# Optimization experiments

Measured on AMD Instinct MI355X. Metric: run time of the kernel, lower is better.

Reference implementation:

```python
import jax, jax.numpy as jnp
import numpy as np

H = 4          # num_heads
EPS = 1e-3     # BatchNorm eps


def conv1x1(x, W, b):
    # x: [B, Cin, N], W: [Cout, Cin], b: [Cout]
    return jnp.einsum('oi,bin->bon', W, x) + b[None, :, None]


def setup_inputs() -> dict:
    key = jax.random.key(0)
    ks = jax.random.split(key, 20)
    B, D, N = 8, 256, 2048
    s = 0.05
    inp = {
        'x': jax.random.normal(ks[0], (B, D, N), jnp.float32),
        'source': jax.random.normal(ks[1], (B, D, N), jnp.float32),
        # attention projections (Conv1d k=1 -> [out, in] weight + bias)
        'Wq': jax.random.normal(ks[2], (D, D), jnp.float32) * s,
        'bq': jax.random.normal(ks[3], (D,), jnp.float32) * s,
        'Wk': jax.random.normal(ks[4], (D, D), jnp.float32) * s,
        'bk': jax.random.normal(ks[5], (D,), jnp.float32) * s,
        'Wv': jax.random.normal(ks[6], (D, D), jnp.float32) * s,
        'bv': jax.random.normal(ks[7], (D,), jnp.float32) * s,
        'Wm': jax.random.normal(ks[8], (D, D), jnp.float32) * s,
        'bm': jax.random.normal(ks[9], (D,), jnp.float32) * s,
        # MLP: [2D -> 2D (BN+ReLU) -> D]
        'W1': jax.random.normal(ks[10], (2 * D, 2 * D), jnp.float32) * s,
        'b1': jax.random.normal(ks[11], (2 * D,), jnp.float32) * s,
        'gamma1': jnp.ones((2 * D,), jnp.float32),
        'beta1': jnp.zeros((2 * D,), jnp.float32),
        'W2': jax.random.normal(ks[12], (D, 2 * D), jnp.float32) * s,
        'b2': jnp.zeros((D,), jnp.float32),  # init.constant_(bias, 0)
    }
    return inp


def reference(x, source, Wq, bq, Wk, bk, Wv, bv, Wm, bm, W1, b1, gamma1, beta1, W2, b2):
    B, D, N = x.shape
    hd = D // H  # head dim; torch view splits channels as (hd, H)
    q = conv1x1(x, Wq, bq).reshape(B, hd, H, N)
    k = conv1x1(source, Wk, bk).reshape(B, hd, H, -1)
    v = conv1x1(source, Wv, bv).reshape(B, hd, H, -1)
    scores = jnp.einsum('bdhn,bdhm->bhnm', q, k) / jnp.sqrt(jnp.float32(hd))
    prob = jax.nn.softmax(scores, axis=-1)
    attn = jnp.einsum('bhnm,bdhm->bdhn', prob, v).reshape(B, D, N)
    message = conv1x1(attn, Wm, bm)
    # MLP on concat([x, message])
    h = conv1x1(jnp.concatenate([x, message], axis=1), W1, b1)  # [B, 2D, N]
    mean = jnp.mean(h, axis=(0, 2), keepdims=True)
    var = jnp.mean((h - mean) ** 2, axis=(0, 2), keepdims=True)  # biased (BN training)
    h = (h - mean) / jnp.sqrt(var + EPS)
    h = h * gamma1[None, :, None] + beta1[None, :, None]
    h = jax.nn.relu(h)
    out = conv1x1(h, W2, b2)  # [B, D, N]
    return out
```

## Files before the change

kernel.cpp:

```cpp
#include <hip/hip_runtime.h>
#include <hip/hip_bf16.h>
#include <math.h>

typedef __bf16 bf16;
typedef __bf16 bf16x4 __attribute__((ext_vector_type(4)));
typedef __bf16 bf16x8 __attribute__((ext_vector_type(8)));
typedef float f32x4 __attribute__((ext_vector_type(4)));

static constexpr int N_TOK = 2048;
static constexpr int B_SZ = 8;

#define MFMA(a, b, c) __builtin_amdgcn_mfma_f32_16x16x32_bf16((a), (b), (c), 0, 0, 0)

__device__ __forceinline__ float fast_exp2(float x) {
  float r;
  asm("v_exp_f32 %0, %1" : "=v"(r) : "v"(x));
  return r;
}

__device__ __host__ __forceinline__ int pi_fwd(int d) {
  return (d & 32) | ((d & 12) << 1) | ((d & 16) >> 2) | (d & 3);
}
__device__ __forceinline__ int pi_inv(int p) {
  return (p & 32) | ((p & 4) << 2) | ((p & 24) >> 1) | (p & 3);
}

__device__ __forceinline__ bf16x4 lo4(bf16x8 v) {
  return __builtin_shufflevector(v, v, 0, 1, 2, 3);
}
__device__ __forceinline__ bf16x4 hi4(bf16x8 v) {
  return __builtin_shufflevector(v, v, 4, 5, 6, 7);
}

__global__ __launch_bounds__(256) void transpose_cvt2(const float* __restrict__ x,
                                                      const float* __restrict__ src,
                                                      bf16* __restrict__ xT,
                                                      bf16* __restrict__ sT) {
  const int z = blockIdx.z;
  const float* in = (z < 8) ? x : src;
  bf16* outT = (z < 8) ? xT : sT;
  const int b = z & 7;
  const int n0 = blockIdx.x * 64, c0 = blockIdx.y * 64;
  const int t = threadIdx.x;
  __shared__ bf16 T[64][72];
  {
    int c = t >> 2, nc = (t & 3) * 16;
    const float* s = in + ((long)b * 256 + c0 + c) * N_TOK + n0 + nc;
#pragma unroll
    for (int q = 0; q < 4; ++q) {
      float4 v = *(const float4*)(s + q * 4);
      T[c][nc + q * 4 + 0] = (bf16)v.x;
      T[c][nc + q * 4 + 1] = (bf16)v.y;
      T[c][nc + q * 4 + 2] = (bf16)v.z;
      T[c][nc + q * 4 + 3] = (bf16)v.w;
    }
  }
  __syncthreads();
  {
    int n = t >> 2, cc = (t & 3) * 16;
    bf16x8 o0, o1;
#pragma unroll
    for (int j = 0; j < 8; ++j) { o0[j] = T[cc + j][n]; o1[j] = T[cc + 8 + j][n]; }
    bf16* dst = outT + ((long)b * N_TOK + n0 + n) * 256 + c0 + cc;
    *(bf16x8*)dst = o0;
    *(bf16x8*)(dst + 8) = o1;
  }
}

__global__ void prep_kernel(const float* __restrict__ Wq, const float* __restrict__ Wk,
                            const float* __restrict__ Wv, const float* __restrict__ Wm,
                            const float* __restrict__ W1, const float* __restrict__ W2,
                            const float* __restrict__ bq, const float* __restrict__ bk,
                            const float* __restrict__ bv,
                            bf16* __restrict__ Wqkv, bf16* __restrict__ Wmp,
                            bf16* __restrict__ W1b, bf16* __restrict__ W2b,
                            float* __restrict__ bqkv) {
  const float SCL = 0.125f * 1.44269504088896340736f;
  int i = blockIdx.x * 256 + threadIdx.x;
  if (i < 65536) {
    int cp = i >> 8, k = i & 255;
    int hh = cp >> 6, pp = cp & 63;
    int d = pi_inv(pp);
    int srcQK = (d * 4 + hh) * 256 + k;
    Wqkv[i] = (bf16)(Wq[srcQK] * SCL);
    Wqkv[65536 + i] = (bf16)Wk[srcQK];
    int srcV = (((cp & 63) << 2) | (cp >> 6)) * 256 + k;
    Wqkv[131072 + i] = (bf16)Wv[srcV];
    int m = i >> 8, c2 = i & 255;
    Wmp[i] = (bf16)Wm[m * 256 + (((c2 & 63) << 2) | (c2 >> 6))];
  } else if (i < 65536 + 262144) {
    int j = i - 65536;
    W1b[j] = (bf16)W1[j];
  } else if (i < 65536 + 262144 + 131072) {
    int j = i - 327680;
    W2b[j] = (bf16)W2[j];
  } else if (i < 65536 + 262144 + 131072 + 256) {
    int c2 = i - 458752;
    int hh = c2 >> 6, pp = c2 & 63;
    int d = pi_inv(pp);
    bqkv[c2] = bq[d * 4 + hh] * SCL;
    bqkv[256 + c2] = bk[d * 4 + hh];
    bqkv[512 + c2] = bv[(c2 & 63) * 4 + (c2 >> 6)];
  }
}

template <int TJ, int MODE>
__global__ __launch_bounds__(256) void gemm_t(
    const bf16* __restrict__ A0, const bf16* __restrict__ A1, int cSplit,
    const bf16* __restrict__ B, long batchB,
    const float* __restrict__ bias, const float2* __restrict__ bnSS,
    bf16* __restrict__ outK, bf16* __restrict__ outV,
    const float2* __restrict__ mlp,
    void* __restrict__ outp, long outR, long batchOut, int K,
    float* __restrict__ psOut, float* __restrict__ pssOut) {
  const int j0 = blockIdx.x * TJ;
  const int i0 = blockIdx.y * 128;
  const int b = blockIdx.z;
  const int t = threadIdx.x;
  const int lane = t & 63, w = t >> 6;
  const int wi = (w >> 1) * 64;
  const int wj = (w & 1) * (TJ / 2);
  const int nl = lane & 15, g = lane >> 4;
  constexpr int FN = TJ / 32;
  constexpr int AsE = 2 * 128 * 40;
  constexpr int BsE = 2 * TJ * 40;
  __shared__ bf16 smem[AsE + BsE];
  auto As = reinterpret_cast<bf16(*)[128][40]>(smem);
  auto Bs = reinterpret_cast<bf16(*)[TJ][40]>(smem + AsE);
  float* redbn = reinterpret_cast<float*>(reinterpret_cast<char*>(smem) +
                                          (AsE + BsE) * 2 - 2048);
  f32x4 acc[4][FN] = {};
  const int asr = t >> 1;
  const int akO = (t & 1) * 16;
  const int abase = (t & 1) * 4;
  const int bsr = (TJ == 128) ? (t >> 1) : (t >> 2);
  const int bq = (TJ == 128) ? (t & 1) : (t & 3);
  const int bbase = (TJ == 128) ? (t & 1) * 4 : ((bq & 1) * 16 + (bq >> 1) * 4);
  const bf16* Bb = B + (long)b * batchB;

  float fL0 = 0, fL1 = 0, fL2 = 0, fL3 = 0;
  int bb = 0, nn = 0;
  if (MODE == 2) {
    int arow = i0 + asr;
    bb = arow >> 11;
    nn = arow & 2047;
#pragma unroll
    for (int h = 0; h < 4; ++h) {
      float2 s0 = mlp[(((long)(bb * 2 + 0) * 4 + h) << 11) + nn];
      float2 s1 = mlp[(((long)(bb * 2 + 1) * 4 + h) << 11) + nn];
      float li = 1.f / (s0.y + s1.y);
      if (h == 0) fL0 = li;
      else if (h == 1) fL1 = li;
      else if (h == 2) fL2 = li;
      else fL3 = li;
    }
  }

  struct Regs { bf16x8 a0, a1, b0, b1; };

  auto loadStep = [&](int s, Regs& R) {
    int ka = s * 32 + akO;
    if (MODE == 1) {
      const bf16* as = ((j0 < 256) ? A0 : A1) + (long)(i0 + asr) * 256 + ka;
      R.a0 = *(const bf16x8*)as;
      R.a1 = *(const bf16x8*)(as + 8);
    } else if (MODE == 2) {
      int h = ka >> 6;
      float li = (h == 0) ? fL0 : (h == 1) ? fL1 : (h == 2) ? fL2 : fL3;
      const bf16* p0 = A0 + ((long)((bb * 2 + 0) * 2048 + nn)) * 256 + ka;
      const bf16* p1 = A0 + ((long)((bb * 2 + 1) * 2048 + nn)) * 256 + ka;
      bf16x8 u0 = *(const bf16x8*)p0, u1 = *(const bf16x8*)(p0 + 8);
      bf16x8 v0 = *(const bf16x8*)p1, v1 = *(const bf16x8*)(p1 + 8);
#pragma unroll
      for (int e = 0; e < 8; ++e) {
        R.a0[e] = (bf16)(((float)u0[e] + (float)v0[e]) * li);
        R.a1[e] = (bf16)(((float)u1[e] + (float)v1[e]) * li);
      }
    } else {
      const bf16* as = (ka < cSplit)
                           ? A0 + (long)(i0 + asr) * cSplit + ka
                           : A1 + (long)(i0 + asr) * (K - cSplit) + (ka - cSplit);
      R.a0 = *(const bf16x8*)as;
      R.a1 = *(const bf16x8*)(as + 8);
    }
    if (TJ == 128) {
      const bf16* bs = Bb + (long)(j0 + bsr) * K + s * 32 + akO;
      R.b0 = *(const bf16x8*)bs;
      R.b1 = *(const bf16x8*)(bs + 8);
    } else {
      R.b0 = *(const bf16x8*)(Bb + (long)(j0 + bsr) * K + s * 32 + bq * 8);
    }
  };
  auto bnApply = [&](bf16x8& r, int kk) {
#pragma unroll
    for (int e = 0; e < 8; ++e) {
      float2 ssv = bnSS[kk + e];
      r[e] = (bf16)fmaxf((float)r[e] * ssv.x + ssv.y, 0.f);
    }
  };
  auto stageStep = [&](int buf, Regs& R, int s) {
    *(bf16x4*)&As[buf][asr][abase] = lo4(R.a0);
    *(bf16x4*)&As[buf][asr][abase + 8] = hi4(R.a0);
    *(bf16x4*)&As[buf][asr][abase + 16] = lo4(R.a1);
    *(bf16x4*)&As[buf][asr][abase + 24] = hi4(R.a1);
    if (TJ == 128) {
      if (MODE == 3) { bnApply(R.b0, s * 32 + akO); bnApply(R.b1, s * 32 + akO + 8); }
      *(bf16x4*)&Bs[buf][bsr][bbase] = lo4(R.b0);
      *(bf16x4*)&Bs[buf][bsr][bbase + 8] = hi4(R.b0);
      *(bf16x4*)&Bs[buf][bsr][bbase + 16] = lo4(R.b1);
      *(bf16x4*)&Bs[buf][bsr][bbase + 24] = hi4(R.b1);
    } else {
      if (MODE == 3) bnApply(R.b0, s * 32 + bq * 8);
      *(bf16x4*)&Bs[buf][bsr][bbase] = lo4(R.b0);
      *(bf16x4*)&Bs[buf][bsr][bbase + 8] = hi4(R.b0);
    }
  };
  auto compute = [&](int buf) {
    bf16x8 af[4], bfr[FN];
#pragma unroll
    for (int fm = 0; fm < 4; ++fm)
      af[fm] = *(const bf16x8*)&As[buf][wi + fm * 16 + nl][g * 8];
#pragma unroll
    for (int fn = 0; fn < FN; ++fn)
      bfr[fn] = *(const bf16x8*)&Bs[buf][wj + fn * 16 + nl][g * 8];
#pragma unroll
    for (int fm = 0; fm < 4; ++fm)
#pragma unroll
      for (int fn = 0; fn < FN; ++fn)
        acc[fm][fn] = MFMA(af[fm], bfr[fn], acc[fm][fn]);
  };

  const int nsteps = K >> 5;
  Regs R0, R1;
  loadStep(0, R0);
  loadStep(1, R1);
  stageStep(0, R0, 0);
  __syncthreads();

  for (int s = 0; s < nsteps; s += 2) {
    if (s + 2 < nsteps) loadStep(s + 2, R0);
    compute(0);
    stageStep(1, R1, s + 1);
    __syncthreads();
    if (s + 3 < nsteps) loadStep(s + 3, R1);
    compute(1);
    if (s + 2 < nsteps) stageStep(0, R0, s + 2);
    __syncthreads();
  }

  const int g4 = g << 2;
  if (MODE == 3) {
    float* outf = (float*)outp;
#pragma unroll
    for (int fm = 0; fm < 4; ++fm)
#pragma unroll
      for (int fn = 0; fn < FN; ++fn)
#pragma unroll
        for (int r = 0; r < 4; ++r) {
          int i = i0 + wi + fm * 16 + g4 + r;
          int j = j0 + wj + fn * 16 + nl;
          outf[(long)b * batchOut + (long)i * outR + j] = acc[fm][fn][r] + bias[i];
        }
  } else {
    constexpr int CW = TJ / 2, CP = CW + 8, TPR = CW / 8;
    auto Ep = reinterpret_cast<bf16(*)[64][CP]>(smem);
    const bool vp = (MODE == 1) && (j0 >= 512);
    float sbn[FN] = {}, ssbn[FN] = {};
#pragma unroll
    for (int fm = 0; fm < 4; ++fm)
#pragma unroll
      for (int fn = 0; fn < FN; ++fn)
#pragma unroll
        for (int r = 0; r < 4; ++r) {
          int il = fm * 16 + g4 + r;
          int jl = fn * 16 + nl;
          float v = acc[fm][fn][r] + bias[j0 + wj + jl];
          if (MODE == 0) { sbn[fn] += v; ssbn[fn] += v * v; }
          if (vp) Ep[w][jl][pi_fwd(il)] = (bf16)v;
          else Ep[w][il][jl] = (bf16)v;
        }
#pragma unroll
    for (int it = 0; it < TPR; ++it) {
      int slot = it * 64 + lane;
      int row = slot / TPR, seg = slot % TPR;
      bf16x8 vv = *(const bf16x8*)&Ep[w][row][seg * 8];
      bf16* dst;
      if (MODE == 1) {
        if (j0 < 512) {
          dst = ((j0 < 256) ? (bf16*)outp : outK) + (long)(i0 + wi + row) * 256 +
                ((j0 + wj) & 255) + seg * 8;
        } else {
          int cch = (j0 - 512) + wj + row;
          dst = outV + ((long)((i0 + wi) >> 11)) * 524288 + (long)cch * 2048 +
                ((i0 + wi) & 2047) + seg * 8;
        }
      } else {
        dst = (bf16*)outp + (long)(i0 + wi + row) * outR + (j0 + wj) + seg * 8;
      }
      *(bf16x8*)dst = vv;
    }
    if constexpr (MODE == 0) {
      if (psOut) {
#pragma unroll
        for (int fn = 0; fn < FN; ++fn) {
#pragma unroll
          for (int xm = 16; xm <= 32; xm <<= 1) {
            sbn[fn] += __shfl_xor(sbn[fn], xm);
            ssbn[fn] += __shfl_xor(ssbn[fn], xm);
          }
        }
        const int wibit = w >> 1, wjbit = w & 1;
        if (g == 0) {
#pragma unroll
          for (int fn = 0; fn < FN; ++fn) {
            redbn[((0 * 2 + wibit) * 2 + wjbit) * 64 + fn * 16 + nl] = sbn[fn];
            redbn[((1 * 2 + wibit) * 2 + wjbit) * 64 + fn * 16 + nl] = ssbn[fn];
          }
        }
        __syncthreads();
        if (t < TJ) {
          int wjb = t >> 6, c = t & 63;
          float su = redbn[((0 * 2 + 0) * 2 + wjb) * 64 + c] +
                     redbn[((0 * 2 + 1) * 2 + wjb) * 64 + c];
          float sq = redbn[((1 * 2 + 0) * 2 + wjb) * 64 + c] +
                     redbn[((1 * 2 + 1) * 2 + wjb) * 64 + c];
          psOut[(long)blockIdx.y * 512 + j0 + t] = su;
          pssOut[(long)blockIdx.y * 512 + j0 + t] = sq;
        }
      }
    }
  }
}

__global__ __launch_bounds__(256) void attn12_kernel(
    const bf16* __restrict__ qT, const bf16* __restrict__ kT,
    const bf16* __restrict__ Vp, bf16* __restrict__ pO, float2* __restrict__ ml) {
  const int id = blockIdx.x;
  const int xcd = id & 7, slot = id >> 3;
  const int pair = (slot >> 4) * 8 + xcd;
  const int n0 = (slot & 15) * 128;
  const int h = pair & 3;
  const int bs = pair >> 2;
  const int b = bs >> 1, split = bs & 1;
  const int t = threadIdx.x, lane = t & 63, w = t >> 6;
  const int nl = lane & 15;
  const int g = lane >> 4, g4 = g << 2;
  __shared__ bf16 Ks[2][64][72], Vs[2][64][72];

  bf16x8 onesv;
#pragma unroll
  for (int j = 0; j < 8; ++j) onesv[j] = (bf16)1.0f;

  bf16x8 qf[2][2];
#pragma unroll
  for (int s2 = 0; s2 < 2; ++s2) {
    const bf16* qrow = qT + ((long)(b * N_TOK + n0 + s2 * 64 + 16 * w + nl)) * 256 + h * 64;
    qf[s2][0] = *(const bf16x8*)(qrow + g * 8);
    qf[s2][1] = *(const bf16x8*)(qrow + 32 + g * 8);
  }

  f32x4 ol[2] = {};
  f32x4 o[2][4] = {};

  const int strow = t >> 2, ste = (t & 3) * 16;
  const bf16* kbase = kT + ((long)(b * N_TOK) + split * 1024 + strow) * 256 + h * 64 + ste;
  const bf16* vbase = Vp + ((long)(b * 256 + h * 64 + strow)) * N_TOK + split * 1024 + ste;

  bf16x8 rk0 = *(const bf16x8*)kbase, rk1 = *(const bf16x8*)(kbase + 8);
  bf16x8 rv0 = *(const bf16x8*)vbase, rv1 = *(const bf16x8*)(vbase + 8);
  *(bf16x8*)&Ks[0][strow][ste] = rk0;
  *(bf16x8*)&Ks[0][strow][ste + 8] = rk1;
  *(bf16x8*)&Vs[0][strow][ste] = rv0;
  *(bf16x8*)&Vs[0][strow][ste + 8] = rv1;
  __syncthreads();

  for (int mt = 0; mt < 16; ++mt) {
    const int cur = mt & 1;
    if (mt < 15) {
      const bf16* kp = kbase + (long)(mt + 1) * 64 * 256;
      const bf16* vp = vbase + (mt + 1) * 64;
      rk0 = *(const bf16x8*)kp;
      rk1 = *(const bf16x8*)(kp + 8);
      rv0 = *(const bf16x8*)vp;
      rv1 = *(const bf16x8*)(vp + 8);
    }

    f32x4 sc0[4], sc1[4];
#pragma unroll
    for (int f = 0; f < 4; ++f) {
      sc0[f] = (f32x4){0.f, 0.f, 0.f, 0.f};
      sc1[f] = (f32x4){0.f, 0.f, 0.f, 0.f};
#pragma unroll
      for (int ks = 0; ks < 2; ++ks) {
        bf16x8 kf = *(const bf16x8*)&Ks[cur][16 * f + nl][ks * 32 + g * 8];
        sc0[f] = MFMA(kf, qf[0][ks], sc0[f]);
        sc1[f] = MFMA(kf, qf[1][ks], sc1[f]);
      }
    }

    bf16x8 pb[2][2];
#pragma unroll
    for (int s2 = 0; s2 < 2; ++s2) {
      f32x4* sc = (s2 == 0) ? sc0 : sc1;
#pragma unroll
      for (int f = 0; f < 4; ++f)
#pragma unroll
        for (int r = 0; r < 4; ++r)
          pb[s2][f >> 1][(f & 1) * 4 + r] = (bf16)fast_exp2(sc[f][r]);
      ol[s2] = MFMA(onesv, pb[s2][0], ol[s2]);
      ol[s2] = MFMA(onesv, pb[s2][1], ol[s2]);
    }

#pragma unroll
    for (int f2 = 0; f2 < 4; ++f2)
#pragma unroll
      for (int ks = 0; ks < 2; ++ks) {
        bf16x8 vf = *(const bf16x8*)&Vs[cur][16 * f2 + nl][ks * 32 + g * 8];
        o[0][f2] = MFMA(vf, pb[0][ks], o[0][f2]);
        o[1][f2] = MFMA(vf, pb[1][ks], o[1][f2]);
      }

    if (mt < 15) {
      *(bf16x8*)&Ks[cur ^ 1][strow][ste] = rk0;
      *(bf16x8*)&Ks[cur ^ 1][strow][ste + 8] = rk1;
      *(bf16x8*)&Vs[cur ^ 1][strow][ste] = rv0;
      *(bf16x8*)&Vs[cur ^ 1][strow][ste + 8] = rv1;
    }
    __syncthreads();
  }

  if (g == 0) {
#pragma unroll
    for (int s2 = 0; s2 < 2; ++s2) {
      int n = n0 + s2 * 64 + 16 * w + nl;
      ml[(((long)bs * 4 + h) << 11) + n] = make_float2(0.f, ol[s2][0]);
    }
  }

#pragma unroll
  for (int f2 = 0; f2 < 4; ++f2)
#pragma unroll
    for (int r = 0; r < 4; ++r) {
      Ks[0][16 * w + nl][16 * f2 + g4 + r] = (bf16)o[0][f2][r];
      Vs[0][16 * w + nl][16 * f2 + g4 + r] = (bf16)o[1][f2][r];
    }
  __syncthreads();
  {
    int rr = lane >> 2, cc = (lane & 3) * 16;
    bf16x8 a0 = *(const bf16x8*)&Ks[0][16 * w + rr][cc];
    bf16x8 a1 = *(const bf16x8*)&Ks[0][16 * w + rr][cc + 8];
    bf16* dst0 = pO + ((long)(bs * N_TOK + n0 + 16 * w + rr)) * 256 + h * 64 + cc;
    *(bf16x8*)dst0 = a0;
    *(bf16x8*)(dst0 + 8) = a1;
    bf16x8 b0 = *(const bf16x8*)&Vs[0][16 * w + rr][cc];
    bf16x8 b1 = *(const bf16x8*)&Vs[0][16 * w + rr][cc + 8];
    bf16* dst1 = pO + ((long)(bs * N_TOK + n0 + 64 + 16 * w + rr)) * 256 + h * 64 + cc;
    *(bf16x8*)dst1 = b0;
    *(bf16x8*)(dst1 + 8) = b1;
  }
}

__global__ __launch_bounds__(256) void bn_finalize(const float* __restrict__ ps,
                                                   const float* __restrict__ pss,
                                                   const float* __restrict__ gamma,
                                                   const float* __restrict__ beta,
                                                   float2* __restrict__ ssbuf) {
  const int j0 = blockIdx.x * 64;
  const int t = threadIdx.x;
  const int c = j0 + (t & 63);
  const int w = t >> 6;
  float s = 0.f, ss = 0.f;
  for (int g = w; g < 128; g += 4) {
    s += ps[(long)g * 512 + c];
    ss += pss[(long)g * 512 + c];
  }
  __shared__ float red[2][4][64];
  red[0][w][t & 63] = s;
  red[1][w][t & 63] = ss;
  __syncthreads();
  if (t < 64) {
    float su = red[0][0][t] + red[0][1][t] + red[0][2][t] + red[0][3][t];
    float sq = red[1][0][t] + red[1][1][t] + red[1][2][t] + red[1][3][t];
    const float invn = 1.f / (float)(B_SZ * N_TOK);
    float mu = su * invn;
    float var = sq * invn - mu * mu;
    float istd = rsqrtf(var + 1e-3f);
    int cc = j0 + t;
    float scl = istd * gamma[cc];
    ssbuf[cc] = make_float2(scl, beta[cc] - mu * scl);
  }
}

extern "C" void kernel_launch(void* const* d_in, const int* in_sizes, int n_in,
                              void* d_out, int out_size, void* d_ws, size_t ws_size,
                              hipStream_t stream) {
  (void)in_sizes; (void)n_in; (void)out_size; (void)ws_size;
  const float* x = (const float*)d_in[0];
  const float* source = (const float*)d_in[1];
  const float* Wq = (const float*)d_in[2];
  const float* bq = (const float*)d_in[3];
  const float* Wk = (const float*)d_in[4];
  const float* bk = (const float*)d_in[5];
  const float* Wv = (const float*)d_in[6];
  const float* bv = (const float*)d_in[7];
  const float* Wm = (const float*)d_in[8];
  const float* bm = (const float*)d_in[9];
  const float* W1 = (const float*)d_in[10];
  const float* b1 = (const float*)d_in[11];
  const float* gamma1 = (const float*)d_in[12];
  const float* beta1 = (const float*)d_in[13];
  const float* W2 = (const float*)d_in[14];
  const float* b2 = (const float*)d_in[15];
  float* out = (float*)d_out;

  char* p = (char*)d_ws;
  size_t off = 0;
  auto alloc = [&](size_t bytes) {
    void* r = p + off;
    off += (bytes + 255) & ~(size_t)255;
    return r;
  };
  const long feat = (long)B_SZ * 256 * N_TOK;
  bf16* xT = (bf16*)alloc(feat * 2);
  bf16* sT = (bf16*)alloc(feat * 2);
  bf16* qT = (bf16*)alloc(feat * 2);
  bf16* kT = (bf16*)alloc(feat * 2);
  bf16* Vp = (bf16*)alloc(feat * 2);
  bf16* mT = (bf16*)alloc(feat * 2);
  bf16* hT = (bf16*)alloc(feat * 4);
  bf16* Wqkv = (bf16*)alloc(768 * 256 * 2);
  bf16* Wmp = (bf16*)alloc(65536 * 2);
  bf16* W1b = (bf16*)alloc(262144 * 2);
  bf16* W2b = (bf16*)alloc(131072 * 2);
  float* bqkv = (float*)alloc(768 * 4);
  float2* ssbuf = (float2*)alloc(512 * 8);
  float* ps = (float*)alloc(512 * 512 * 4);
  float* pss = (float*)alloc(512 * 512 * 4);

  bf16* pO = hT;
  float2* mlbuf = (float2*)ps;

  dim3 blk(256);
  transpose_cvt2<<<dim3(32, 4, 16), blk, 0, stream>>>(x, source, xT, sT);
  prep_kernel<<<1794, blk, 0, stream>>>(Wq, Wk, Wv, Wm, W1, W2, bq, bk, bv,
                                        Wqkv, Wmp, W1b, W2b, bqkv);

  gemm_t<128, 1><<<dim3(6, 128, 1), blk, 0, stream>>>(
      xT, sT, 256, Wqkv, 0, bqkv, nullptr, kT, Vp, nullptr, qT, 256, 0, 256,
      nullptr, nullptr);

  attn12_kernel<<<dim3(1024, 1, 1), blk, 0, stream>>>(qT, kT, Vp, pO, mlbuf);

  gemm_t<64, 2><<<dim3(4, 128, 1), blk, 0, stream>>>(
      pO, nullptr, 256, Wmp, 0, bm, nullptr, nullptr, nullptr, mlbuf, mT, 256, 0, 256,
      nullptr, nullptr);
  gemm_t<128, 0><<<dim3(4, 128, 1), blk, 0, stream>>>(
      xT, mT, 256, W1b, 0, b1, nullptr, nullptr, nullptr, nullptr, hT, 512, 0, 512,
      ps, pss);

  bn_finalize<<<8, blk, 0, stream>>>(ps, pss, gamma1, beta1, ssbuf);

  gemm_t<64, 3><<<dim3(32, 2, 8), blk, 0, stream>>>(
      W2b, nullptr, 512, hT, (long)N_TOK * 512, b2, ssbuf, nullptr, nullptr, nullptr,
      out, N_TOK, (long)256 * N_TOK, 512, nullptr, nullptr);
}
```

Measured before the change: 147.7 us.

## Load K/V MFMA fragments directly from global memory, dropping LDS staging

```diff
diff --git a/kernel.cpp b/kernel.cpp
--- a/kernel.cpp
+++ b/kernel.cpp
@@ -332,7 +332,7 @@
   }
 }
 
-__global__ __launch_bounds__(256) void attn12_kernel(
+__global__ __launch_bounds__(256) void attn15_kernel(
     const bf16* __restrict__ qT, const bf16* __restrict__ kT,
     const bf16* __restrict__ Vp, bf16* __restrict__ pO, float2* __restrict__ ml) {
   const int id = blockIdx.x;
@@ -345,7 +345,7 @@
   const int t = threadIdx.x, lane = t & 63, w = t >> 6;
   const int nl = lane & 15;
   const int g = lane >> 4, g4 = g << 2;
-  __shared__ bf16 Ks[2][64][72], Vs[2][64][72];
+  __shared__ bf16 Ep[2][4][16][72];
 
   bf16x8 onesv;
 #pragma unroll
@@ -362,28 +362,11 @@
   f32x4 ol[2] = {};
   f32x4 o[2][4] = {};
 
-  const int strow = t >> 2, ste = (t & 3) * 16;
-  const bf16* kbase = kT + ((long)(b * N_TOK) + split * 1024 + strow) * 256 + h * 64 + ste;
-  const bf16* vbase = Vp + ((long)(b * 256 + h * 64 + strow)) * N_TOK + split * 1024 + ste;
-
-  bf16x8 rk0 = *(const bf16x8*)kbase, rk1 = *(const bf16x8*)(kbase + 8);
-  bf16x8 rv0 = *(const bf16x8*)vbase, rv1 = *(const bf16x8*)(vbase + 8);
-  *(bf16x8*)&Ks[0][strow][ste] = rk0;
-  *(bf16x8*)&Ks[0][strow][ste + 8] = rk1;
-  *(bf16x8*)&Vs[0][strow][ste] = rv0;
-  *(bf16x8*)&Vs[0][strow][ste + 8] = rv1;
-  __syncthreads();
+  const bf16* kB = kT + ((long)(b * N_TOK + split * 1024 + nl)) * 256 + h * 64 + g * 8;
+  const bf16* vB = Vp + ((long)(b * 256 + h * 64 + nl)) * N_TOK + split * 1024 + g * 8;
 
   for (int mt = 0; mt < 16; ++mt) {
-    const int cur = mt & 1;
-    if (mt < 15) {
-      const bf16* kp = kbase + (long)(mt + 1) * 64 * 256;
-      const bf16* vp = vbase + (mt + 1) * 64;
-      rk0 = *(const bf16x8*)kp;
-      rk1 = *(const bf16x8*)(kp + 8);
-      rv0 = *(const bf16x8*)vp;
-      rv1 = *(const bf16x8*)(vp + 8);
-    }
+    const bf16* kt0 = kB + (long)mt * 64 * 256;
 
     f32x4 sc0[4], sc1[4];
 #pragma unroll
@@ -392,7 +375,7 @@
       sc1[f] = (f32x4){0.f, 0.f, 0.f, 0.f};
 #pragma unroll
       for (int ks = 0; ks < 2; ++ks) {
-        bf16x8 kf = *(const bf16x8*)&Ks[cur][16 * f + nl][ks * 32 + g * 8];
+        bf16x8 kf = *(const bf16x8*)(kt0 + f * 16 * 256 + ks * 32);
         sc0[f] = MFMA(kf, qf[0][ks], sc0[f]);
         sc1[f] = MFMA(kf, qf[1][ks], sc1[f]);
       }
@@ -415,18 +398,10 @@
     for (int f2 = 0; f2 < 4; ++f2)
 #pragma unroll
       for (int ks = 0; ks < 2; ++ks) {
-        bf16x8 vf = *(const bf16x8*)&Vs[cur][16 * f2 + nl][ks * 32 + g * 8];
+        bf16x8 vf = *(const bf16x8*)(vB + (long)f2 * 16 * N_TOK + mt * 64 + ks * 32);
         o[0][f2] = MFMA(vf, pb[0][ks], o[0][f2]);
         o[1][f2] = MFMA(vf, pb[1][ks], o[1][f2]);
       }
-
-    if (mt < 15) {
-      *(bf16x8*)&Ks[cur ^ 1][strow][ste] = rk0;
-      *(bf16x8*)&Ks[cur ^ 1][strow][ste + 8] = rk1;
-      *(bf16x8*)&Vs[cur ^ 1][strow][ste] = rv0;
-      *(bf16x8*)&Vs[cur ^ 1][strow][ste + 8] = rv1;
-    }
-    __syncthreads();
   }
 
   if (g == 0) {
@@ -441,22 +416,20 @@
   for (int f2 = 0; f2 < 4; ++f2)
 #pragma unroll
     for (int r = 0; r < 4; ++r) {
-      Ks[0][16 * w + nl][16 * f2 + g4 + r] = (bf16)o[0][f2][r];
-      Vs[0][16 * w + nl][16 * f2 + g4 + r] = (bf16)o[1][f2][r];
+      Ep[0][w][nl][16 * f2 + g4 + r] = (bf16)o[0][f2][r];
+      Ep[1][w][nl][16 * f2 + g4 + r] = (bf16)o[1][f2][r];
     }
   __syncthreads();
   {
     int rr = lane >> 2, cc = (lane & 3) * 16;
-    bf16x8 a0 = *(const bf16x8*)&Ks[0][16 * w + rr][cc];
-    bf16x8 a1 = *(const bf16x8*)&Ks[0][16 * w + rr][cc + 8];
-    bf16* dst0 = pO + ((long)(bs * N_TOK + n0 + 16 * w + rr)) * 256 + h * 64 + cc;
-    *(bf16x8*)dst0 = a0;
-    *(bf16x8*)(dst0 + 8) = a1;
-    bf16x8 b0 = *(const bf16x8*)&Vs[0][16 * w + rr][cc];
-    bf16x8 b1 = *(const bf16x8*)&Vs[0][16 * w + rr][cc + 8];
-    bf16* dst1 = pO + ((long)(bs * N_TOK + n0 + 64 + 16 * w + rr)) * 256 + h * 64 + cc;
-    *(bf16x8*)dst1 = b0;
-    *(bf16x8*)(dst1 + 8) = b1;
+#pragma unroll
+    for (int s2 = 0; s2 < 2; ++s2) {
+      bf16x8 a0 = *(const bf16x8*)&Ep[s2][w][rr][cc];
+      bf16x8 a1 = *(const bf16x8*)&Ep[s2][w][rr][cc + 8];
+      bf16* dst = pO + ((long)(bs * N_TOK + n0 + s2 * 64 + 16 * w + rr)) * 256 + h * 64 + cc;
+      *(bf16x8*)dst = a0;
+      *(bf16x8*)(dst + 8) = a1;
+    }
   }
 }
 
@@ -549,7 +522,7 @@
       xT, sT, 256, Wqkv, 0, bqkv, nullptr, kT, Vp, nullptr, qT, 256, 0, 256,
       nullptr, nullptr);
 
-  attn12_kernel<<<dim3(1024, 1, 1), blk, 0, stream>>>(qT, kT, Vp, pO, mlbuf);
+  attn15_kernel<<<dim3(1024, 1, 1), blk, 0, stream>>>(qT, kT, Vp, pO, mlbuf);
 
   gemm_t<64, 2><<<dim3(4, 128, 1), blk, 0, stream>>>(
       pO, nullptr, 256, Wmp, 0, bm, nullptr, nullptr, nullptr, mlbuf, mT, 256, 0, 256,
```

Result: slower. 223.2 us (+51.2%).
